# Performance work log

Hardware: AMD Instinct MI355X
Metric: run time of the kernel (lower is better)

## Reference

```python
import jax, jax.numpy as jnp
import numpy as np

N = 50000          # nodes
E = 640000         # edges (before self-loops)
DIM_FEATS = 128
DIM_H = 32
HEADS1 = 8
NUM_CLASS = 16
NEG_SLOPE_ATT = 0.2   # PyG GATv2Conv default negative_slope
NEG_SLOPE_OUT = 0.01  # F.leaky_relu default


def setup_inputs() -> dict:
    key = jax.random.key(0)
    ks = jax.random.split(key, 12)
    s = 0.1
    x = jax.random.normal(ks[0], (N, DIM_FEATS), dtype=jnp.float32)
    edge_index = jax.random.randint(ks[1], (2, E), 0, N, dtype=jnp.int32)
    # GATv2Conv layer 1: dim_feats -> dim_h per head, 8 heads, concat
    W1l = jax.random.normal(ks[2], (DIM_FEATS, HEADS1 * DIM_H), dtype=jnp.float32) * s
    W1r = jax.random.normal(ks[3], (DIM_FEATS, HEADS1 * DIM_H), dtype=jnp.float32) * s
    att1 = jax.random.normal(ks[4], (HEADS1, DIM_H), dtype=jnp.float32) * s
    b1 = jnp.zeros((HEADS1 * DIM_H,), dtype=jnp.float32)
    # GATv2Conv layer 2: 256 -> num_class, 1 head, concat=False
    W2l = jax.random.normal(ks[5], (HEADS1 * DIM_H, NUM_CLASS), dtype=jnp.float32) * s
    W2r = jax.random.normal(ks[6], (HEADS1 * DIM_H, NUM_CLASS), dtype=jnp.float32) * s
    att2 = jax.random.normal(ks[7], (1, NUM_CLASS), dtype=jnp.float32) * s
    b2 = jnp.zeros((NUM_CLASS,), dtype=jnp.float32)
    return {"x": x, "edge_index": edge_index, "W1l": W1l, "W1r": W1r,
            "att1": att1, "b1": b1, "W2l": W2l, "W2r": W2r,
            "att2": att2, "b2": b2}


def _segment_softmax(scores, seg, num_segments):
    # scores: [E, H], seg: [E] destination node ids
    m = jax.ops.segment_max(scores, seg, num_segments=num_segments)  # [N, H]
    e = jnp.exp(scores - m[seg])
    denom = jax.ops.segment_sum(e, seg, num_segments=num_segments)   # [N, H]
    return e / (denom[seg] + 1e-16)


def _gatv2_layer(x, src, dst, Wl, Wr, att, bias, heads, out_ch, concat):
    n = x.shape[0]
    xl = (x @ Wl).reshape(n, heads, out_ch)  # source transform
    xr = (x @ Wr).reshape(n, heads, out_ch)  # target transform
    # per-edge GATv2 score: a^T LeakyReLU(xl[j] + xr[i])
    e = jax.nn.leaky_relu(xl[src] + xr[dst], negative_slope=NEG_SLOPE_ATT)  # [E,H,F]
    alpha = jnp.einsum('ehf,hf->eh', e, att)                                # [E,H]
    alpha = _segment_softmax(alpha, dst, n)
    msg = xl[src] * alpha[:, :, None]                                       # [E,H,F]
    out = jax.ops.segment_sum(msg, dst, num_segments=n)                     # [N,H,F]
    out = out.reshape(n, heads * out_ch) if concat else out.mean(axis=1)
    return out + bias


def reference(x, edge_index, W1l, W1r, att1, b1, W2l, W2r, att2, b2):
    # add_self_loops=True (PyG GATv2Conv default)
    loop = jnp.arange(N, dtype=edge_index.dtype)
    src = jnp.concatenate([edge_index[0], loop])
    dst = jnp.concatenate([edge_index[1], loop])
    # eval mode: all dropouts are identity
    h = _gatv2_layer(x, src, dst, W1l, W1r, att1, b1, HEADS1, DIM_H, concat=True)
    h = jax.nn.elu(h)
    h = _gatv2_layer(h, src, dst, W2l, W2r, att2, b2, 1, NUM_CLASS, concat=False)
    return jax.nn.leaky_relu(h, negative_slope=NEG_SLOPE_OUT)
```

## Files before the change

kernel.cpp:

```cpp
#include <hip/hip_runtime.h>
#include <math.h>

#define NN 50000
#define E0 640000
#define ET 690000
#define F1 128
#define D1 256
#define C2 16
#define NB 196
#define MPAD 50048
#define PADK 136
#define LOG2E 1.4426950408889634f
#define NBK1 782

typedef _Float16 f16x8 __attribute__((ext_vector_type(8)));
typedef _Float16 h2 __attribute__((ext_vector_type(2)));
typedef __attribute__((ext_vector_type(4))) float f32x4;

__device__ __forceinline__ unsigned short f2h(float f) {
  union { _Float16 h; unsigned short u; } c;
  c.h = (_Float16)f;
  return c.u;
}
__device__ __forceinline__ float h2f(unsigned short u) {
  union { unsigned short u; _Float16 h; } c; c.u = u; return (float)c.h;
}
__device__ __forceinline__ h2 u2h2(unsigned u) {
  union { unsigned u; h2 h; } c; c.u = u; return c.h;
}
__device__ __forceinline__ unsigned h22u(h2 h) {
  union { h2 h; unsigned u; } c; c.h = h; return c.u;
}

template <int CTRL>
__device__ __forceinline__ float dpp_add(float c) {
  int t = __builtin_amdgcn_update_dpp(0, __builtin_bit_cast(int, c), CTRL, 0xF, 0xF, true);
  return c + __builtin_bit_cast(float, t);
}
template <int K>
__device__ __forceinline__ int dpp_bcast(int v) {
  constexpr int ctrl = K | (K << 2) | (K << 4) | (K << 6);
  return __builtin_amdgcn_update_dpp(0, v, ctrl, 0xF, 0xF, true);
}

__global__ __launch_bounds__(256) void k_prep(
    const float* __restrict__ Wl, const float* __restrict__ Wr,
    const float* __restrict__ W2l, const float* __restrict__ W2r,
    const int* __restrict__ ei,
    unsigned short* __restrict__ wt, unsigned short* __restrict__ wt2,
    int* __restrict__ deg) {
  const int b = blockIdx.x;
  if (b < 256) {
    int tid = b * 256 + threadIdx.x;
    int n = tid >> 7, k = tid & 127;
    float v = (n < 256) ? Wl[k * 256 + n] : Wr[k * 256 + (n - 256)];
    wt[tid] = f2h(v);
  } else if (b < 288) {
    int tid = (b - 256) * 256 + threadIdx.x;
    int n = tid >> 8, k = tid & 255;
    float v = (n < 16) ? W2l[k * 16 + n] : W2r[k * 16 + (n - 16)];
    wt2[tid] = f2h(v);
  } else {
    int e = (b - 288) * 256 + threadIdx.x;
    if (e >= ET) return;
    int d = (e < E0) ? ei[E0 + e] : (e - E0);
    atomicAdd(&deg[d], 1);
  }
}

__global__ __launch_bounds__(256) void k_gemm1m(
    const float* __restrict__ x, const unsigned short* __restrict__ wt,
    unsigned short* __restrict__ xlh, unsigned short* __restrict__ xrh) {
  __shared__ unsigned short Al[64 * PADK];
  __shared__ unsigned short Bl[128 * PADK];
  const int t = threadIdx.x;
  const int m0 = blockIdx.x * 64;
  {
    const int r = t >> 4;
    const int c = (t & 15) * 8;
#pragma unroll
    for (int p = 0; p < 4; ++p) {
      const int row = r + p * 16;
      const int rg = m0 + row;
      const float* xp = &x[(size_t)(rg < NN ? rg : NN - 1) * F1 + c];
      float4 lo = *(const float4*)xp;
      float4 hi = *(const float4*)(xp + 4);
      h2 q0 = h2{(_Float16)lo.x, (_Float16)lo.y};
      h2 q1 = h2{(_Float16)lo.z, (_Float16)lo.w};
      h2 q2 = h2{(_Float16)hi.x, (_Float16)hi.y};
      h2 q3 = h2{(_Float16)hi.z, (_Float16)hi.w};
      uint4 st; st.x = h22u(q0); st.y = h22u(q1); st.z = h22u(q2); st.w = h22u(q3);
      *(uint4*)&Al[row * PADK + c] = st;
    }
  }
  const int wave = t >> 6, lane = t & 63;
  const int mw = (wave >> 1) * 32, nw = (wave & 1) * 64;
  const int fr = lane & 15, fq = lane >> 4;
  for (int ny = 0; ny < 4; ++ny) {
    const int n0 = ny * 128;
    {
      const int r = t >> 4;
      const int c = (t & 15) * 8;
#pragma unroll
      for (int p = 0; p < 8; ++p) {
        const int row = r + p * 16;
        *(float4*)&Bl[row * PADK + c] = *(const float4*)&wt[(size_t)(n0 + row) * F1 + c];
      }
    }
    __syncthreads();
    f32x4 acc[2][4] = {};
#pragma unroll
    for (int ks = 0; ks < 4; ++ks) {
      const int ko = ks * 32 + fq * 8;
      f16x8 a[2], b[4];
#pragma unroll
      for (int i = 0; i < 2; ++i)
        a[i] = *(const f16x8*)&Al[(mw + i * 16 + fr) * PADK + ko];
#pragma unroll
      for (int j = 0; j < 4; ++j)
        b[j] = *(const f16x8*)&Bl[(nw + j * 16 + fr) * PADK + ko];
#pragma unroll
      for (int i = 0; i < 2; ++i)
#pragma unroll
        for (int j = 0; j < 4; ++j)
          acc[i][j] = __builtin_amdgcn_mfma_f32_16x16x32_f16(a[i], b[j], acc[i][j], 0, 0, 0);
    }
    __syncthreads();
    unsigned short* outp = (n0 < 256) ? xlh : xrh;
    const int cb = (n0 & 255) + nw + fr;
#pragma unroll
    for (int j = 0; j < 4; ++j) {
      const int col = cb + j * 16;
      const int head = col >> 5, f = col & 31;
      unsigned short* hp = outp + (size_t)head * NN * 32 + f;
#pragma unroll
      for (int i = 0; i < 2; ++i) {
        const int gm0 = m0 + mw + i * 16 + fq * 4;
#pragma unroll
        for (int r = 0; r < 4; ++r) {
          const int gm = gm0 + r;
          if (gm < NN) hp[(size_t)gm * 32] = f2h(acc[i][j][r]);
        }
      }
    }
  }
}

__global__ __launch_bounds__(256) void k_scan_part(const int* __restrict__ deg,
                                                   int* __restrict__ part) {
  int i = blockIdx.x * 256 + threadIdx.x;
  int v = (i < NN) ? deg[i] : 0;
  v += __shfl_xor(v, 1);  v += __shfl_xor(v, 2);  v += __shfl_xor(v, 4);
  v += __shfl_xor(v, 8);  v += __shfl_xor(v, 16); v += __shfl_xor(v, 32);
  __shared__ int w[4];
  if ((threadIdx.x & 63) == 0) w[threadIdx.x >> 6] = v;
  __syncthreads();
  if (threadIdx.x == 0) part[blockIdx.x] = w[0] + w[1] + w[2] + w[3];
}

__global__ __launch_bounds__(256) void k_scan_apply(int* __restrict__ deg,
                                                    const int* __restrict__ part,
                                                    int* __restrict__ offs) {
  __shared__ int lds[256];
  __shared__ int red[4];
  const int b = blockIdx.x, t = threadIdx.x;
  const int i = b * 256 + t;
  int v = (i < NN) ? deg[i] : 0;
  lds[t] = v;
  int pp = 0;
  for (int j = t; j < b; j += 256) pp += part[j];
  pp += __shfl_xor(pp, 1);  pp += __shfl_xor(pp, 2);  pp += __shfl_xor(pp, 4);
  pp += __shfl_xor(pp, 8);  pp += __shfl_xor(pp, 16); pp += __shfl_xor(pp, 32);
  if ((t & 63) == 0) red[t >> 6] = pp;
  __syncthreads();
  const int prefix = red[0] + red[1] + red[2] + red[3];
  for (int off = 1; off < 256; off <<= 1) {
    int u = (t >= off) ? lds[t - off] : 0;
    __syncthreads();
    lds[t] += u;
    __syncthreads();
  }
  int excl = prefix + lds[t] - v;
  if (i < NN) { offs[i] = excl; deg[i] = excl; }
  if (b == NB - 1 && t == 255) offs[NN] = prefix + lds[255];
}

__global__ void k_scatter(const int* __restrict__ ei, int* __restrict__ cur,
                          unsigned short* __restrict__ csr) {
  int e = blockIdx.x * 256 + threadIdx.x;
  if (e >= ET) return;
  int s, d;
  if (e < E0) { s = ei[e]; d = ei[E0 + e]; } else { s = d = e - E0; }
  int pos = atomicAdd(&cur[d], 1);
  csr[pos] = (unsigned short)s;
}

__global__ __launch_bounds__(256) void k_agg1(
    const unsigned short* __restrict__ xlh, const unsigned short* __restrict__ xrh,
    unsigned short* __restrict__ hb,
    const int* __restrict__ offs, const unsigned short* __restrict__ csr,
    const float* __restrict__ att, const float* __restrict__ b1) {
  const int b = blockIdx.x;
  const int head = b & 7;
  const int wave = threadIdx.x >> 6;
  const int lane = threadIdx.x & 63;
  const int g = lane >> 2;
  const int j4 = lane & 3;
  const int idxn = (b >> 3) * 64 + wave * 16 + g;
  const bool valid = idxn < NN;
  const int n = valid ? idxn : 0;
  const int colh = j4 * 8;
  const int col = head * 32 + colh;
  const unsigned short* xlhead = xlh + (size_t)head * NN * 32;

  const uint4 xru = *(const uint4*)&xrh[((size_t)head * NN + n) * 32 + colh];
  h2 xr2[4];
  xr2[0] = u2h2(xru.x); xr2[1] = u2h2(xru.y);
  xr2[2] = u2h2(xru.z); xr2[3] = u2h2(xru.w);
  float at8[8];
  *(float4*)&at8[0] = *(const float4*)&att[col];
  *(float4*)&at8[4] = *(const float4*)&att[col + 4];
  h2 ath6[4], ath4[4];
#pragma unroll
  for (int j = 0; j < 4; ++j) {
    ath6[j] = h2{(_Float16)(at8[2 * j] * (0.6f * LOG2E)),
                 (_Float16)(at8[2 * j + 1] * (0.6f * LOG2E))};
    ath4[j] = h2{(_Float16)(at8[2 * j] * (0.4f * LOG2E)),
                 (_Float16)(at8[2 * j + 1] * (0.4f * LOG2E))};
  }
  float l = 0.f;
  h2 acc2[4] = {h2{0, 0}, h2{0, 0}, h2{0, 0}, h2{0, 0}};
  const int beg = valid ? offs[n] : 0;
  const int fin = valid ? offs[n + 1] : 0;

  auto ldids = [&](int base) -> int {
    int a = base + j4;
    a = (a < fin) ? a : beg;
    return (int)csr[a];
  };
  auto XLrow = [&](int s) -> uint4 {
    return *(const uint4*)&xlhead[(size_t)s * 32 + colh];
  };
  auto edge = [&](const uint4& w, bool live) {
    h2 xh[4];
    xh[0] = u2h2(w.x); xh[1] = u2h2(w.y); xh[2] = u2h2(w.z); xh[3] = u2h2(w.w);
    float cv = 0.f, ca = 0.f;
#pragma unroll
    for (int j = 0; j < 4; ++j) {
      h2 v = xh[j] + xr2[j];
      h2 a = u2h2(h22u(v) & 0x7FFF7FFFu);
      cv = __builtin_amdgcn_fdot2(v, ath6[j], cv, false);
      ca = __builtin_amdgcn_fdot2(a, ath4[j], ca, false);
    }
    float c = cv + ca;
    c = dpp_add<0xB1>(c);
    c = dpp_add<0x4E>(c);
    float p = exp2f(c);
    p = live ? p : 0.f;
    l += p;
    const _Float16 ph = (_Float16)p;
    const h2 p2 = h2{ph, ph};
#pragma unroll
    for (int j = 0; j < 4; ++j) acc2[j] += p2 * xh[j];
  };

  int ids = ldids(beg);
  uint4 w0 = XLrow(dpp_bcast<0>(ids));
  uint4 w1 = XLrow(dpp_bcast<1>(ids));
  uint4 w2 = XLrow(dpp_bcast<2>(ids));
  uint4 w3 = XLrow(dpp_bcast<3>(ids));
  int ids1 = ldids(beg + 4);
  for (int idx = beg; idx < fin; idx += 4) {
    const uint4 v0 = XLrow(dpp_bcast<0>(ids1));
    const uint4 v1 = XLrow(dpp_bcast<1>(ids1));
    const uint4 v2 = XLrow(dpp_bcast<2>(ids1));
    const uint4 v3 = XLrow(dpp_bcast<3>(ids1));
    const int ids2 = ldids(idx + 8);
    edge(w0, true);
    edge(w1, idx + 1 < fin);
    edge(w2, idx + 2 < fin);
    edge(w3, idx + 3 < fin);
    w0 = v0; w1 = v1; w2 = v2; w3 = v3; ids1 = ids2;
  }

  if (valid) {
    const float rl = __builtin_amdgcn_rcpf(l + 1e-16f);
    float b8[8], o[8];
    *(float4*)&b8[0] = *(const float4*)&b1[col];
    *(float4*)&b8[4] = *(const float4*)&b1[col + 4];
#pragma unroll
    for (int j = 0; j < 4; ++j) {
      o[2 * j]     = (float)acc2[j][0] * rl + b8[2 * j];
      o[2 * j + 1] = (float)acc2[j][1] * rl + b8[2 * j + 1];
    }
#pragma unroll
    for (int k = 0; k < 8; ++k)
      o[k] = o[k] > 0.f ? o[k] : exp2f(o[k] * LOG2E) - 1.f;
    ushort4 p;
    p.x = f2h(o[0]); p.y = f2h(o[1]); p.z = f2h(o[2]); p.w = f2h(o[3]);
    ushort4 q;
    q.x = f2h(o[4]); q.y = f2h(o[5]); q.z = f2h(o[6]); q.w = f2h(o[7]);
    uint4 packed;
    packed.x = *(unsigned*)&p.x; packed.y = *(unsigned*)&p.z;
    packed.z = *(unsigned*)&q.x; packed.w = *(unsigned*)&q.z;
    *(uint4*)&hb[(size_t)n * D1 + col] = packed;
  }
}

__global__ __launch_bounds__(256) void k_gemm2m(
    const unsigned short* __restrict__ hb, const unsigned short* __restrict__ wt2,
    unsigned short* __restrict__ h2lh, float* __restrict__ h2r) {
  const int t = threadIdx.x;
  const int wave = t >> 6, lane = t & 63;
  const int fr = lane & 15, fq = lane >> 4;
  const int m0 = blockIdx.x * 128 + wave * 32;
  f32x4 acc[2][2] = {};
#pragma unroll
  for (int ks = 0; ks < 8; ++ks) {
    const int ko = ks * 32 + fq * 8;
    f16x8 a[2], b[2];
#pragma unroll
    for (int i = 0; i < 2; ++i) {
      int row = m0 + i * 16 + fr; if (row >= NN) row = NN - 1;
      a[i] = *(const f16x8*)&hb[(size_t)row * D1 + ko];
    }
#pragma unroll
    for (int j = 0; j < 2; ++j)
      b[j] = *(const f16x8*)&wt2[(j * 16 + fr) * 256 + ko];
#pragma unroll
    for (int i = 0; i < 2; ++i)
#pragma unroll
      for (int j = 0; j < 2; ++j)
        acc[i][j] = __builtin_amdgcn_mfma_f32_16x16x32_f16(a[i], b[j], acc[i][j], 0, 0, 0);
  }
#pragma unroll
  for (int i = 0; i < 2; ++i) {
    const int gm0 = m0 + i * 16 + fq * 4;
#pragma unroll
    for (int r = 0; r < 4; ++r) {
      const int gm = gm0 + r;
      if (gm < NN) {
        h2lh[(size_t)gm * C2 + fr] = f2h(acc[i][0][r]);
        h2r[(size_t)gm * C2 + fr] = acc[i][1][r];
      }
    }
  }
}

__global__ __launch_bounds__(256) void k_agg2(
    const unsigned short* __restrict__ h2lh, const float* __restrict__ h2r,
    const int* __restrict__ offs, const unsigned short* __restrict__ csr,
    const float* __restrict__ att2, const float* __restrict__ b2,
    float* __restrict__ out) {
  const int wave = threadIdx.x >> 6;
  const int lane = threadIdx.x & 63;
  const int n = blockIdx.x * 4 + wave;
  if (n >= NN) return;
  const int c = lane & 15, g = lane >> 4;
  const float xr_v = h2r[(size_t)n * C2 + c];
  const float att_v = att2[c] * LOG2E;
  float l = 0.f, acc = 0.f;
  const int beg = offs[n], fin = offs[n + 1];
  for (int idx = beg + g; idx < fin; idx += 8) {
    const int i1 = idx + 4;
    const bool m1 = i1 < fin;
    const int s0 = csr[idx];
    const int s1 = csr[m1 ? i1 : idx];
    const float xl0 = h2f(h2lh[(size_t)s0 * C2 + c]);
    const float xl1 = h2f(h2lh[(size_t)s1 * C2 + c]);
    float v0 = xl0 + xr_v; v0 = fmaxf(v0, 0.2f * v0);
    float v1 = xl1 + xr_v; v1 = fmaxf(v1, 0.2f * v1);
    float sc0 = v0 * att_v, sc1 = v1 * att_v;
    sc0 = dpp_add<0xB1>(sc0);   sc1 = dpp_add<0xB1>(sc1);
    sc0 = dpp_add<0x4E>(sc0);   sc1 = dpp_add<0x4E>(sc1);
    sc0 = dpp_add<0x124>(sc0);  sc1 = dpp_add<0x124>(sc1);
    sc0 = dpp_add<0x128>(sc0);  sc1 = dpp_add<0x128>(sc1);
    const float p0 = exp2f(sc0);
    const float p1 = m1 ? exp2f(sc1) : 0.f;
    l += p0 + p1;
    acc = fmaf(p0, xl0, fmaf(p1, xl1, acc));
  }
  l += __shfl_xor(l, 16);   l += __shfl_xor(l, 32);
  acc += __shfl_xor(acc, 16); acc += __shfl_xor(acc, 32);
  float o = acc * __builtin_amdgcn_rcpf(l + 1e-16f) + b2[c];
  o = o > 0.f ? o : 0.01f * o;
  if (lane < 16) out[(size_t)n * C2 + c] = o;
}

extern "C" void kernel_launch(void* const* d_in, const int* in_sizes, int n_in,
                              void* d_out, int out_size, void* d_ws, size_t ws_size,
                              hipStream_t stream) {
  const float* x    = (const float*)d_in[0];
  const int*   ei   = (const int*)d_in[1];
  const float* W1l  = (const float*)d_in[2];
  const float* W1r  = (const float*)d_in[3];
  const float* att1 = (const float*)d_in[4];
  const float* b1   = (const float*)d_in[5];
  const float* W2l  = (const float*)d_in[6];
  const float* W2r  = (const float*)d_in[7];
  const float* att2 = (const float*)d_in[8];
  const float* b2   = (const float*)d_in[9];
  float* out = (float*)d_out;

  unsigned short* xlh = (unsigned short*)d_ws;
  unsigned short* xrh = xlh + (size_t)NN * D1;
  unsigned short* hb  = xrh + (size_t)NN * D1;
  int* deg  = (int*)(hb + (size_t)NN * D1);
  int* part = deg + NN;
  int* offs = part + NB;
  unsigned short* csr = (unsigned short*)(offs + NN + 1);
  unsigned short* wt  = csr + ET + 2;
  unsigned short* wt2 = wt + 512 * F1;
  unsigned short* h2lh = xlh;
  float* h2r = (float*)(h2lh + (size_t)NN * C2);

  hipMemsetAsync(deg, 0, NN * sizeof(int), stream);
  k_prep<<<288 + (ET + 255) / 256, 256, 0, stream>>>(
      W1l, W1r, W2l, W2r, ei, wt, wt2, deg);
  k_gemm1m<<<MPAD / 64, 256, 0, stream>>>(x, wt, xlh, xrh);
  k_scan_part<<<NB, 256, 0, stream>>>(deg, part);
  k_scan_apply<<<NB, 256, 0, stream>>>(deg, part, offs);
  k_scatter<<<(ET + 255) / 256, 256, 0, stream>>>(ei, deg, csr);
  k_agg1<<<NBK1 * 8, 256, 0, stream>>>(xlh, xrh, hb, offs, csr, att1, b1);
  k_gemm2m<<<(NN + 127) / 128, 256, 0, stream>>>(hb, wt2, h2lh, h2r);
  k_agg2<<<NN / 4, 256, 0, stream>>>(h2lh, h2r, offs, csr, att2, b2, out);
}
```

Baseline: 256.9 us.

## Fuse CSR edge scatter into layer-1 GEMM launch and pack per-node offsets

```diff
diff --git a/kernel.cpp b/kernel.cpp
--- a/kernel.cpp
+++ b/kernel.cpp
@@ -12,6 +12,7 @@
 #define PADK 136
 #define LOG2E 1.4426950408889634f
 #define NBK1 782
+#define GEMMB 782
 
 typedef _Float16 f16x8 __attribute__((ext_vector_type(8)));
 typedef _Float16 h2 __attribute__((ext_vector_type(2)));
@@ -68,84 +69,6 @@
   }
 }
 
-__global__ __launch_bounds__(256) void k_gemm1m(
-    const float* __restrict__ x, const unsigned short* __restrict__ wt,
-    unsigned short* __restrict__ xlh, unsigned short* __restrict__ xrh) {
-  __shared__ unsigned short Al[64 * PADK];
-  __shared__ unsigned short Bl[128 * PADK];
-  const int t = threadIdx.x;
-  const int m0 = blockIdx.x * 64;
-  {
-    const int r = t >> 4;
-    const int c = (t & 15) * 8;
-#pragma unroll
-    for (int p = 0; p < 4; ++p) {
-      const int row = r + p * 16;
-      const int rg = m0 + row;
-      const float* xp = &x[(size_t)(rg < NN ? rg : NN - 1) * F1 + c];
-      float4 lo = *(const float4*)xp;
-      float4 hi = *(const float4*)(xp + 4);
-      h2 q0 = h2{(_Float16)lo.x, (_Float16)lo.y};
-      h2 q1 = h2{(_Float16)lo.z, (_Float16)lo.w};
-      h2 q2 = h2{(_Float16)hi.x, (_Float16)hi.y};
-      h2 q3 = h2{(_Float16)hi.z, (_Float16)hi.w};
-      uint4 st; st.x = h22u(q0); st.y = h22u(q1); st.z = h22u(q2); st.w = h22u(q3);
-      *(uint4*)&Al[row * PADK + c] = st;
-    }
-  }
-  const int wave = t >> 6, lane = t & 63;
-  const int mw = (wave >> 1) * 32, nw = (wave & 1) * 64;
-  const int fr = lane & 15, fq = lane >> 4;
-  for (int ny = 0; ny < 4; ++ny) {
-    const int n0 = ny * 128;
-    {
-      const int r = t >> 4;
-      const int c = (t & 15) * 8;
-#pragma unroll
-      for (int p = 0; p < 8; ++p) {
-        const int row = r + p * 16;
-        *(float4*)&Bl[row * PADK + c] = *(const float4*)&wt[(size_t)(n0 + row) * F1 + c];
-      }
-    }
-    __syncthreads();
-    f32x4 acc[2][4] = {};
-#pragma unroll
-    for (int ks = 0; ks < 4; ++ks) {
-      const int ko = ks * 32 + fq * 8;
-      f16x8 a[2], b[4];
-#pragma unroll
-      for (int i = 0; i < 2; ++i)
-        a[i] = *(const f16x8*)&Al[(mw + i * 16 + fr) * PADK + ko];
-#pragma unroll
-      for (int j = 0; j < 4; ++j)
-        b[j] = *(const f16x8*)&Bl[(nw + j * 16 + fr) * PADK + ko];
-#pragma unroll
-      for (int i = 0; i < 2; ++i)
-#pragma unroll
-        for (int j = 0; j < 4; ++j)
-          acc[i][j] = __builtin_amdgcn_mfma_f32_16x16x32_f16(a[i], b[j], acc[i][j], 0, 0, 0);
-    }
-    __syncthreads();
-    unsigned short* outp = (n0 < 256) ? xlh : xrh;
-    const int cb = (n0 & 255) + nw + fr;
-#pragma unroll
-    for (int j = 0; j < 4; ++j) {
-      const int col = cb + j * 16;
-      const int head = col >> 5, f = col & 31;
-      unsigned short* hp = outp + (size_t)head * NN * 32 + f;
-#pragma unroll
-      for (int i = 0; i < 2; ++i) {
-        const int gm0 = m0 + mw + i * 16 + fq * 4;
-#pragma unroll
-        for (int r = 0; r < 4; ++r) {
-          const int gm = gm0 + r;
-          if (gm < NN) hp[(size_t)gm * 32] = f2h(acc[i][j][r]);
-        }
-      }
-    }
-  }
-}
-
 __global__ __launch_bounds__(256) void k_scan_part(const int* __restrict__ deg,
                                                    int* __restrict__ part) {
   int i = blockIdx.x * 256 + threadIdx.x;
@@ -160,7 +83,9 @@
 
 __global__ __launch_bounds__(256) void k_scan_apply(int* __restrict__ deg,
                                                     const int* __restrict__ part,
-                                                    int* __restrict__ offs) {
+                                                    int* __restrict__ offs,
+                                                    uint2* __restrict__ ninfo,
+                                                    unsigned short* __restrict__ csr) {
   __shared__ int lds[256];
   __shared__ int red[4];
   const int b = blockIdx.x, t = threadIdx.x;
@@ -181,24 +106,108 @@
     __syncthreads();
   }
   int excl = prefix + lds[t] - v;
-  if (i < NN) { offs[i] = excl; deg[i] = excl; }
+  if (i < NN) {
+    offs[i] = excl;
+    deg[i] = excl + 1;
+    csr[excl] = (unsigned short)i;
+    ninfo[i] = make_uint2((unsigned)excl, (unsigned)i | ((unsigned)v << 16));
+  }
   if (b == NB - 1 && t == 255) offs[NN] = prefix + lds[255];
 }
 
-__global__ void k_scatter(const int* __restrict__ ei, int* __restrict__ cur,
-                          unsigned short* __restrict__ csr) {
-  int e = blockIdx.x * 256 + threadIdx.x;
-  if (e >= ET) return;
-  int s, d;
-  if (e < E0) { s = ei[e]; d = ei[E0 + e]; } else { s = d = e - E0; }
-  int pos = atomicAdd(&cur[d], 1);
-  csr[pos] = (unsigned short)s;
+__global__ __launch_bounds__(256) void k_gemm1s(
+    const float* __restrict__ x, const unsigned short* __restrict__ wt,
+    unsigned short* __restrict__ xlh, unsigned short* __restrict__ xrh,
+    const int* __restrict__ ei, int* __restrict__ cur,
+    unsigned short* __restrict__ csr) {
+  __shared__ unsigned short Al[64 * PADK];
+  __shared__ unsigned short Bl[128 * PADK];
+  if (blockIdx.x >= GEMMB) {
+    int e = (blockIdx.x - GEMMB) * 256 + threadIdx.x;
+    if (e < E0) {
+      int s = ei[e], d = ei[E0 + e];
+      int pos = atomicAdd(&cur[d], 1);
+      csr[pos] = (unsigned short)s;
+    }
+    return;
+  }
+  const int t = threadIdx.x;
+  const int m0 = blockIdx.x * 64;
+  {
+    const int r = t >> 4;
+    const int c = (t & 15) * 8;
+#pragma unroll
+    for (int p = 0; p < 4; ++p) {
+      const int row = r + p * 16;
+      const int rg = m0 + row;
+      const float* xp = &x[(size_t)(rg < NN ? rg : NN - 1) * F1 + c];
+      float4 lo = *(const float4*)xp;
+      float4 hi = *(const float4*)(xp + 4);
+      h2 q0 = h2{(_Float16)lo.x, (_Float16)lo.y};
+      h2 q1 = h2{(_Float16)lo.z, (_Float16)lo.w};
+      h2 q2 = h2{(_Float16)hi.x, (_Float16)hi.y};
+      h2 q3 = h2{(_Float16)hi.z, (_Float16)hi.w};
+      uint4 st; st.x = h22u(q0); st.y = h22u(q1); st.z = h22u(q2); st.w = h22u(q3);
+      *(uint4*)&Al[row * PADK + c] = st;
+    }
+  }
+  const int wave = t >> 6, lane = t & 63;
+  const int mw = (wave >> 1) * 32, nw = (wave & 1) * 64;
+  const int fr = lane & 15, fq = lane >> 4;
+  for (int ny = 0; ny < 4; ++ny) {
+    const int n0 = ny * 128;
+    {
+      const int r = t >> 4;
+      const int c = (t & 15) * 8;
+#pragma unroll
+      for (int p = 0; p < 8; ++p) {
+        const int row = r + p * 16;
+        *(float4*)&Bl[row * PADK + c] = *(const float4*)&wt[(size_t)(n0 + row) * F1 + c];
+      }
+    }
+    __syncthreads();
+    f32x4 acc[2][4] = {};
+#pragma unroll
+    for (int ks = 0; ks < 4; ++ks) {
+      const int ko = ks * 32 + fq * 8;
+      f16x8 a[2], b[4];
+#pragma unroll
+      for (int i = 0; i < 2; ++i)
+        a[i] = *(const f16x8*)&Al[(mw + i * 16 + fr) * PADK + ko];
+#pragma unroll
+      for (int j = 0; j < 4; ++j)
+        b[j] = *(const f16x8*)&Bl[(nw + j * 16 + fr) * PADK + ko];
+#pragma unroll
+      for (int i = 0; i < 2; ++i)
+#pragma unroll
+        for (int j = 0; j < 4; ++j)
+          acc[i][j] = __builtin_amdgcn_mfma_f32_16x16x32_f16(a[i], b[j], acc[i][j], 0, 0, 0);
+    }
+    __syncthreads();
+    unsigned short* outp = (n0 < 256) ? xlh : xrh;
+    const int cb = (n0 & 255) + nw + fr;
+#pragma unroll
+    for (int j = 0; j < 4; ++j) {
+      const int col = cb + j * 16;
+      const int head = col >> 5, f = col & 31;
+      unsigned short* hp = outp + (size_t)head * NN * 32 + f;
+#pragma unroll
+      for (int i = 0; i < 2; ++i) {
+        const int gm0 = m0 + mw + i * 16 + fq * 4;
+#pragma unroll
+        for (int r = 0; r < 4; ++r) {
+          const int gm = gm0 + r;
+          if (gm < NN) hp[(size_t)gm * 32] = f2h(acc[i][j][r]);
+        }
+      }
+    }
+  }
 }
 
 __global__ __launch_bounds__(256) void k_agg1(
     const unsigned short* __restrict__ xlh, const unsigned short* __restrict__ xrh,
     unsigned short* __restrict__ hb,
-    const int* __restrict__ offs, const unsigned short* __restrict__ csr,
+    const uint2* __restrict__ ninfo, const unsigned short* __restrict__ csr,
     const float* __restrict__ att, const float* __restrict__ b1) {
   const int b = blockIdx.x;
   const int head = b & 7;
@@ -213,6 +222,10 @@
   const int col = head * 32 + colh;
   const unsigned short* xlhead = xlh + (size_t)head * NN * 32;
 
+  const uint2 nf = ninfo[n];
+  const int beg = (int)nf.x;
+  const int fin = valid ? beg + (int)(nf.y >> 16) : beg;
+
   const uint4 xru = *(const uint4*)&xrh[((size_t)head * NN + n) * 32 + colh];
   h2 xr2[4];
   xr2[0] = u2h2(xru.x); xr2[1] = u2h2(xru.y);
@@ -230,8 +243,6 @@
   }
   float l = 0.f;
   h2 acc2[4] = {h2{0, 0}, h2{0, 0}, h2{0, 0}, h2{0, 0}};
-  const int beg = valid ? offs[n] : 0;
-  const int fin = valid ? offs[n + 1] : 0;
 
   auto ldids = [&](int base) -> int {
     int a = base + j4;
@@ -408,7 +419,8 @@
   int* deg  = (int*)(hb + (size_t)NN * D1);
   int* part = deg + NN;
   int* offs = part + NB;
-  unsigned short* csr = (unsigned short*)(offs + NN + 1);
+  uint2* ninfo = (uint2*)(offs + NN + 2);
+  unsigned short* csr = (unsigned short*)(ninfo + NN);
   unsigned short* wt  = csr + ET + 2;
   unsigned short* wt2 = wt + 512 * F1;
   unsigned short* h2lh = xlh;
@@ -417,11 +429,11 @@
   hipMemsetAsync(deg, 0, NN * sizeof(int), stream);
   k_prep<<<288 + (ET + 255) / 256, 256, 0, stream>>>(
       W1l, W1r, W2l, W2r, ei, wt, wt2, deg);
-  k_gemm1m<<<MPAD / 64, 256, 0, stream>>>(x, wt, xlh, xrh);
   k_scan_part<<<NB, 256, 0, stream>>>(deg, part);
-  k_scan_apply<<<NB, 256, 0, stream>>>(deg, part, offs);
-  k_scatter<<<(ET + 255) / 256, 256, 0, stream>>>(ei, deg, csr);
-  k_agg1<<<NBK1 * 8, 256, 0, stream>>>(xlh, xrh, hb, offs, csr, att1, b1);
+  k_scan_apply<<<NB, 256, 0, stream>>>(deg, part, offs, ninfo, csr);
+  k_gemm1s<<<GEMMB + (E0 + 255) / 256, 256, 0, stream>>>(
+      x, wt, xlh, xrh, ei, deg, csr);
+  k_agg1<<<NBK1 * 8, 256, 0, stream>>>(xlh, xrh, hb, ninfo, csr, att1, b1);
   k_gemm2m<<<(NN + 127) / 128, 256, 0, stream>>>(hb, wt2, h2lh, h2r);
   k_agg2<<<NN / 4, 256, 0, stream>>>(h2lh, h2r, offs, csr, att2, b2, out);
 }
```

Result: no change. 261.8 us (+1.9%).
